# Optimization experiments

Hardware: AMD Instinct MI355X
Metric: run time of the kernel (lower is better)

## Reference

```python
import jax, jax.numpy as jnp
import numpy as np

LN_EPS = 1e-5


def setup_inputs() -> dict:
    key = jax.random.key(0)
    k_h, k_s, k_d, k_w = jax.random.split(key, 4)
    N, E, F_IN, F_OUT = 100000, 1600000, 128, 128
    h = jax.random.normal(k_h, (N, F_IN), dtype=jnp.float32)
    src = jax.random.randint(k_s, (E,), 0, N, dtype=jnp.int32)
    dst = jax.random.randint(k_d, (E,), 0, N, dtype=jnp.int32)
    # Linear(2*in_feats, out_feats): weight [out, 2*in], bias [out]
    W = jax.random.normal(k_w, (F_OUT, 2 * F_IN), dtype=jnp.float32) * (1.0 / np.sqrt(2 * F_IN))
    b = jnp.zeros((F_OUT,), dtype=jnp.float32)
    gamma = jnp.ones((F_OUT,), dtype=jnp.float32)
    beta = jnp.zeros((F_OUT,), dtype=jnp.float32)
    return {"h": h, "src": src, "dst": dst, "W": W, "b": b, "gamma": gamma, "beta": beta}


def reference(h, src, dst, W, b, gamma, beta):
    N = h.shape[0]
    # mean aggregation: update_all(copy_src('h','m'), mean('m','h'))
    msg_sum = jax.ops.segment_sum(h[src], dst, num_segments=N)          # [N, F]
    deg = jax.ops.segment_sum(jnp.ones_like(dst, dtype=h.dtype), dst, num_segments=N)  # [N]
    ah = msg_sum / jnp.maximum(deg, 1.0)[:, None]                        # zero-degree -> 0 (DGL mean gives 0)
    # concat + linear
    hc = jnp.concatenate([h, ah], axis=1)                                # [N, 2F]
    z = hc @ W.T + b                                                     # [N, out]
    # LayerNorm (elementwise affine)
    mu = jnp.mean(z, axis=-1, keepdims=True)
    var = jnp.mean((z - mu) ** 2, axis=-1, keepdims=True)
    z = (z - mu) * jax.lax.rsqrt(var + LN_EPS) * gamma + beta
    # activation = relu
    return jax.nn.relu(z)
```

## Files before the change

### kernel.cpp

```cpp
#include <hip/hip_runtime.h>
#include <stdint.h>

#define FDIM 128
#define NBITS 7
#define BNODES 128
#define CAP 3072
#define PBATCH 8192

typedef __attribute__((ext_vector_type(8))) short bf16x8;
typedef __attribute__((ext_vector_type(4))) float f32x4;
typedef __attribute__((ext_vector_type(8))) unsigned short u16x8;

__device__ __forceinline__ unsigned short f32_to_bf16(float f) {
  union { float f; uint32_t u; } v; v.f = f;
  uint32_t u = v.u;
  u += 0x7FFFu + ((u >> 16) & 1u);
  return (unsigned short)(u >> 16);
}
__device__ __forceinline__ float bf16_to_f32(unsigned short h) {
  union { uint32_t u; float f; } v; v.u = ((uint32_t)h) << 16;
  return v.f;
}

__device__ __forceinline__ void gload_lds16(const void* g, void* l) {
  __builtin_amdgcn_global_load_lds(
      (const __attribute__((address_space(1))) void*)g,
      (__attribute__((address_space(3))) void*)l, 16, 0, 0);
}

__global__ void zero_i32(int* p, int n) {
  int i = blockIdx.x * blockDim.x + threadIdx.x;
  if (i < n) p[i] = 0;
}

__global__ void cvt_bf16_8(const float* __restrict__ in, unsigned short* __restrict__ o, int n8) {
  int i = blockIdx.x * blockDim.x + threadIdx.x;
  if (i >= n8) return;
  float4 a = ((const float4*)in)[i * 2], b = ((const float4*)in)[i * 2 + 1];
  u16x8 r;
  r[0] = f32_to_bf16(a.x); r[1] = f32_to_bf16(a.y); r[2] = f32_to_bf16(a.z); r[3] = f32_to_bf16(a.w);
  r[4] = f32_to_bf16(b.x); r[5] = f32_to_bf16(b.y); r[6] = f32_to_bf16(b.z); r[7] = f32_to_bf16(b.w);
  ((u16x8*)o)[i] = r;
}

__global__ __launch_bounds__(256) void partition_edges(
    const int* __restrict__ src, const int* __restrict__ dst,
    int* __restrict__ gcur, int2* __restrict__ pairs, int E, int nbk) {
  __shared__ int hist[800];
  for (int k = threadIdx.x; k < nbk; k += 256) hist[k] = 0;
  __syncthreads();
  int base = blockIdx.x * PBATCH;
#pragma unroll
  for (int j = 0; j < PBATCH / 256; ++j) {
    int i = base + j * 256 + threadIdx.x;
    if (i < E) atomicAdd(&hist[dst[i] >> NBITS], 1);
  }
  __syncthreads();
  for (int k = threadIdx.x; k < nbk; k += 256) {
    int c = hist[k];
    hist[k] = (c > 0) ? atomicAdd(&gcur[k], c) : 0;
  }
  __syncthreads();
#pragma unroll
  for (int j = 0; j < PBATCH / 256; ++j) {
    int i = base + j * 256 + threadIdx.x;
    if (i < E) {
      int d = dst[i];
      int b = d >> NBITS;
      int pos = atomicAdd(&hist[b], 1);
      if (pos < CAP) pairs[(size_t)b * CAP + pos] = make_int2(src[i], d);
    }
  }
}

__global__ __launch_bounds__(256) void sort_aggregate(
    const unsigned short* __restrict__ h2, const int* __restrict__ gcur,
    const int2* __restrict__ pairs, unsigned short* __restrict__ ah2, int N) {
  __shared__ int cnt[BNODES];
  __shared__ int off[BNODES];
  __shared__ int cur[BNODES];
  __shared__ int lsrc[CAP];
  int b = blockIdx.x;
  int n0 = b << NBITS;
  int tid = threadIdx.x;
  int ec = gcur[b]; if (ec > CAP) ec = CAP;
  for (int k = tid; k < BNODES; k += 256) cnt[k] = 0;
  __syncthreads();
  const int2* pb = pairs + (size_t)b * CAP;
  for (int e = tid; e < ec; e += 256) atomicAdd(&cnt[pb[e].y & (BNODES - 1)], 1);
  __syncthreads();
  if (tid < BNODES) off[tid] = cnt[tid];
  __syncthreads();
  for (int s = 1; s < BNODES; s <<= 1) {
    int v = 0;
    if (tid < BNODES && tid >= s) v = off[tid - s];
    __syncthreads();
    if (tid < BNODES) off[tid] += v;
    __syncthreads();
  }
  if (tid < BNODES) { int e0 = off[tid] - cnt[tid]; off[tid] = e0; cur[tid] = e0; }
  __syncthreads();
  for (int e = tid; e < ec; e += 256) {
    int2 p = pb[e];
    int pos = atomicAdd(&cur[p.y & (BNODES - 1)], 1);
    lsrc[pos] = p.x;
  }
  __syncthreads();
  int g = tid >> 4, lane = tid & 15;
  for (int ln = g; ln < BNODES; ln += 16) {
    int node = n0 + ln;
    if (node >= N) break;
    int s0 = off[ln], d = cnt[ln];
    float acc[8] = {0.f, 0.f, 0.f, 0.f, 0.f, 0.f, 0.f, 0.f};
    for (int e = s0; e < s0 + d; ++e) {
      int sn = lsrc[e];
      u16x8 v = *(const u16x8*)(h2 + (size_t)sn * 128 + lane * 8);
#pragma unroll
      for (int j = 0; j < 8; ++j) acc[j] += bf16_to_f32(v[j]);
    }
    float inv = 1.0f / (float)(d > 0 ? d : 1);
    u16x8 r;
#pragma unroll
    for (int j = 0; j < 8; ++j) r[j] = f32_to_bf16(acc[j] * inv);
    *(u16x8*)(ah2 + (size_t)node * 128 + lane * 8) = r;
  }
}

__global__ __launch_bounds__(256) void gemm_mfma_ln_relu(
    const unsigned short* __restrict__ h2, const unsigned short* __restrict__ ah2,
    const unsigned short* __restrict__ W2, const float* __restrict__ bias,
    const float* __restrict__ gamma, const float* __restrict__ beta,
    float* __restrict__ out, int N) {
  __shared__ unsigned short As[128 * 64];
  __shared__ unsigned short Ws[128 * 64];
  int tid = threadIdx.x;
  int w = tid >> 6, l = tid & 63;
  int lr = l & 15, lg = l >> 4;
  int n0 = blockIdx.x * 128;

  f32x4 acc[2][8];
#pragma unroll
  for (int rt = 0; rt < 2; ++rt)
#pragma unroll
    for (int ct = 0; ct < 8; ++ct) acc[rt][ct] = (f32x4){0.f, 0.f, 0.f, 0.f};

  for (int kt = 0; kt < 4; ++kt) {
    const unsigned short* abase = (kt < 2) ? h2 : ah2;
#pragma unroll
    for (int rd = 0; rd < 4; ++rd) {
      int off = rd * 4096 + tid * 16;
      int r = off >> 7;
      int s = (off >> 4) & 7;
      int ls = s ^ (r & 7);
      int gn = n0 + r; if (gn > N - 1) gn = N - 1;
      gload_lds16((const char*)abase + (size_t)gn * 256 + (size_t)(kt & 1) * 128 + ls * 16,
                  (char*)As + off);
      gload_lds16((const char*)W2 + (size_t)r * 512 + (size_t)kt * 128 + ls * 16,
                  (char*)Ws + off);
    }
    __syncthreads();

    bf16x8 aF[2][2], bF[8][2];
#pragma unroll
    for (int rt = 0; rt < 2; ++rt)
#pragma unroll
      for (int kc = 0; kc < 2; ++kc) {
        int r = w * 32 + rt * 16 + lr;
        int slot = kc * 4 + lg;
        aF[rt][kc] = *(const bf16x8*)((const char*)As + r * 128 + ((slot ^ (r & 7)) * 16));
      }
#pragma unroll
    for (int ct = 0; ct < 8; ++ct)
#pragma unroll
      for (int kc = 0; kc < 2; ++kc) {
        int r = ct * 16 + lr;
        int slot = kc * 4 + lg;
        bF[ct][kc] = *(const bf16x8*)((const char*)Ws + r * 128 + ((slot ^ (r & 7)) * 16));
      }
#pragma unroll
    for (int rt = 0; rt < 2; ++rt)
#pragma unroll
      for (int ct = 0; ct < 8; ++ct)
#pragma unroll
        for (int kc = 0; kc < 2; ++kc)
          acc[rt][ct] = __builtin_amdgcn_mfma_f32_16x16x32_bf16(
              aF[rt][kc], bF[ct][kc], acc[rt][ct], 0, 0, 0);
    __syncthreads();
  }

  float bj[8], gj[8], tj[8];
#pragma unroll
  for (int ct = 0; ct < 8; ++ct) {
    int c = ct * 16 + lr;
    bj[ct] = bias[c]; gj[ct] = gamma[c]; tj[ct] = beta[c];
  }
#pragma unroll
  for (int rt = 0; rt < 2; ++rt)
#pragma unroll
    for (int q = 0; q < 4; ++q) {
      int n = n0 + w * 32 + rt * 16 + lg * 4 + q;
      float v[8], s = 0.f, s2 = 0.f;
#pragma unroll
      for (int ct = 0; ct < 8; ++ct) {
        v[ct] = acc[rt][ct][q] + bj[ct];
        s += v[ct]; s2 += v[ct] * v[ct];
      }
#pragma unroll
      for (int off = 1; off < 16; off <<= 1) {
        s  += __shfl_xor(s, off);
        s2 += __shfl_xor(s2, off);
      }
      float mean = s * (1.f / 128.f);
      float var = s2 * (1.f / 128.f) - mean * mean;
      float rstd = rsqrtf(var + 1e-5f);
      if (n < N) {
#pragma unroll
        for (int ct = 0; ct < 8; ++ct) {
          float o = (v[ct] - mean) * rstd * gj[ct] + tj[ct];
          out[(size_t)n * FDIM + ct * 16 + lr] = fmaxf(o, 0.f);
        }
      }
    }
}

extern "C" void kernel_launch(void* const* d_in, const int* in_sizes, int n_in,
                              void* d_out, int out_size, void* d_ws, size_t ws_size,
                              hipStream_t stream) {
  const float* h     = (const float*)d_in[0];
  const int*   src   = (const int*)d_in[1];
  const int*   dst   = (const int*)d_in[2];
  const float* W     = (const float*)d_in[3];
  const float* bias  = (const float*)d_in[4];
  const float* gamma = (const float*)d_in[5];
  const float* beta  = (const float*)d_in[6];
  float* out = (float*)d_out;
  int N = in_sizes[0] / FDIM;
  int E = in_sizes[1];
  int nbk = (N + BNODES - 1) >> NBITS;

  int* gcur = (int*)d_ws;
  int2* pairs = (int2*)((char*)d_ws + 4096);
  unsigned short* h2  = (unsigned short*)((char*)pairs + (size_t)nbk * CAP * 8);
  unsigned short* ah2 = h2 + (size_t)N * 128;
  unsigned short* W2  = ah2 + (size_t)N * 128;

  zero_i32<<<(nbk + 255) / 256, 256, 0, stream>>>(gcur, nbk);
  cvt_bf16_8<<<(N * FDIM / 8 + 255) / 256, 256, 0, stream>>>(h, h2, N * FDIM / 8);
  cvt_bf16_8<<<(FDIM * 2 * FDIM / 8 + 255) / 256, 256, 0, stream>>>(W, W2, FDIM * 2 * FDIM / 8);
  partition_edges<<<(E + PBATCH - 1) / PBATCH, 256, 0, stream>>>(src, dst, gcur, pairs, E, nbk);
  sort_aggregate<<<nbk, 256, 0, stream>>>(h2, gcur, pairs, ah2, N);
  gemm_mfma_ln_relu<<<(N + 127) / 128, 256, 0, stream>>>(h2, ah2, W2, bias, gamma, beta, out, N);
}
```

Measured before the change: 270.0 us.

## Pack edge pairs into 32-bit words, shrink buckets, vectorize partition, unroll gather

Halves the bucket size to 64 nodes and packs each edge's source id and local destination into one 32-bit word, halving the traffic for the partitioned pairs. The partition kernel reads src/dst as int4 vectors, and the aggregation loop gathers four neighbor rows at a time into independent accumulators to raise memory-level parallelism. This adds more aggregation blocks and a larger shared histogram. The packing relies on node ids fitting in 26 bits, and the vector loads assume 16-byte aligned edge arrays.

After: 224.6 us. 1.2x faster.

```diff
diff --git a/kernel.cpp b/kernel.cpp
--- a/kernel.cpp
+++ b/kernel.cpp
@@ -2,9 +2,9 @@
 #include <stdint.h>
 
 #define FDIM 128
-#define NBITS 7
-#define BNODES 128
-#define CAP 3072
+#define NBITS 6
+#define BNODES 64
+#define CAP 1536
 #define PBATCH 8192
 
 typedef __attribute__((ext_vector_type(8))) short bf16x8;
@@ -45,15 +45,25 @@
 
 __global__ __launch_bounds__(256) void partition_edges(
     const int* __restrict__ src, const int* __restrict__ dst,
-    int* __restrict__ gcur, int2* __restrict__ pairs, int E, int nbk) {
-  __shared__ int hist[800];
+    int* __restrict__ gcur, unsigned int* __restrict__ pairs, int E, int nbk) {
+  __shared__ int hist[1600];
   for (int k = threadIdx.x; k < nbk; k += 256) hist[k] = 0;
   __syncthreads();
   int base = blockIdx.x * PBATCH;
-#pragma unroll
-  for (int j = 0; j < PBATCH / 256; ++j) {
-    int i = base + j * 256 + threadIdx.x;
-    if (i < E) atomicAdd(&hist[dst[i] >> NBITS], 1);
+  const int4* d4p = (const int4*)(dst + base);
+  const int4* s4p = (const int4*)(src + base);
+  int nvec = PBATCH / 4;
+#pragma unroll
+  for (int j = 0; j < PBATCH / 1024; ++j) {
+    int vi = j * 256 + threadIdx.x;
+    int i0 = base + vi * 4;
+    if (i0 < E) {
+      int4 d = d4p[vi];
+      atomicAdd(&hist[d.x >> NBITS], 1);
+      if (i0 + 1 < E) atomicAdd(&hist[d.y >> NBITS], 1);
+      if (i0 + 2 < E) atomicAdd(&hist[d.z >> NBITS], 1);
+      if (i0 + 3 < E) atomicAdd(&hist[d.w >> NBITS], 1);
+    }
   }
   __syncthreads();
   for (int k = threadIdx.x; k < nbk; k += 256) {
@@ -62,20 +72,29 @@
   }
   __syncthreads();
 #pragma unroll
-  for (int j = 0; j < PBATCH / 256; ++j) {
-    int i = base + j * 256 + threadIdx.x;
-    if (i < E) {
-      int d = dst[i];
-      int b = d >> NBITS;
-      int pos = atomicAdd(&hist[b], 1);
-      if (pos < CAP) pairs[(size_t)b * CAP + pos] = make_int2(src[i], d);
+  for (int j = 0; j < PBATCH / 1024; ++j) {
+    int vi = j * 256 + threadIdx.x;
+    int i0 = base + vi * 4;
+    if (i0 < E) {
+      int4 d = d4p[vi];
+      int4 s = s4p[vi];
+#pragma unroll
+      for (int q = 0; q < 4; ++q) {
+        if (i0 + q >= E) break;
+        int dd = (q == 0) ? d.x : (q == 1) ? d.y : (q == 2) ? d.z : d.w;
+        int ss = (q == 0) ? s.x : (q == 1) ? s.y : (q == 2) ? s.z : s.w;
+        int b = dd >> NBITS;
+        int pos = atomicAdd(&hist[b], 1);
+        if (pos < CAP)
+          pairs[(size_t)b * CAP + pos] = ((unsigned)ss << NBITS) | (unsigned)(dd & (BNODES - 1));
+      }
     }
   }
 }
 
 __global__ __launch_bounds__(256) void sort_aggregate(
     const unsigned short* __restrict__ h2, const int* __restrict__ gcur,
-    const int2* __restrict__ pairs, unsigned short* __restrict__ ah2, int N) {
+    const unsigned int* __restrict__ pairs, unsigned short* __restrict__ ah2, int N) {
   __shared__ int cnt[BNODES];
   __shared__ int off[BNODES];
   __shared__ int cur[BNODES];
@@ -84,10 +103,10 @@
   int n0 = b << NBITS;
   int tid = threadIdx.x;
   int ec = gcur[b]; if (ec > CAP) ec = CAP;
-  for (int k = tid; k < BNODES; k += 256) cnt[k] = 0;
-  __syncthreads();
-  const int2* pb = pairs + (size_t)b * CAP;
-  for (int e = tid; e < ec; e += 256) atomicAdd(&cnt[pb[e].y & (BNODES - 1)], 1);
+  if (tid < BNODES) cnt[tid] = 0;
+  __syncthreads();
+  const unsigned int* pb = pairs + (size_t)b * CAP;
+  for (int e = tid; e < ec; e += 256) atomicAdd(&cnt[pb[e] & (BNODES - 1)], 1);
   __syncthreads();
   if (tid < BNODES) off[tid] = cnt[tid];
   __syncthreads();
@@ -101,9 +120,9 @@
   if (tid < BNODES) { int e0 = off[tid] - cnt[tid]; off[tid] = e0; cur[tid] = e0; }
   __syncthreads();
   for (int e = tid; e < ec; e += 256) {
-    int2 p = pb[e];
-    int pos = atomicAdd(&cur[p.y & (BNODES - 1)], 1);
-    lsrc[pos] = p.x;
+    unsigned int p = pb[e];
+    int pos = atomicAdd(&cur[p & (BNODES - 1)], 1);
+    lsrc[pos] = (int)(p >> NBITS);
   }
   __syncthreads();
   int g = tid >> 4, lane = tid & 15;
@@ -111,17 +130,30 @@
     int node = n0 + ln;
     if (node >= N) break;
     int s0 = off[ln], d = cnt[ln];
-    float acc[8] = {0.f, 0.f, 0.f, 0.f, 0.f, 0.f, 0.f, 0.f};
-    for (int e = s0; e < s0 + d; ++e) {
-      int sn = lsrc[e];
-      u16x8 v = *(const u16x8*)(h2 + (size_t)sn * 128 + lane * 8);
-#pragma unroll
-      for (int j = 0; j < 8; ++j) acc[j] += bf16_to_f32(v[j]);
+    int e = s0, eend = s0 + d;
+    float a0[8] = {0,0,0,0,0,0,0,0}, a1[8] = {0,0,0,0,0,0,0,0};
+    float a2[8] = {0,0,0,0,0,0,0,0}, a3[8] = {0,0,0,0,0,0,0,0};
+    for (; e + 4 <= eend; e += 4) {
+      u16x8 v0 = *(const u16x8*)(h2 + (size_t)lsrc[e]     * 128 + lane * 8);
+      u16x8 v1 = *(const u16x8*)(h2 + (size_t)lsrc[e + 1] * 128 + lane * 8);
+      u16x8 v2 = *(const u16x8*)(h2 + (size_t)lsrc[e + 2] * 128 + lane * 8);
+      u16x8 v3 = *(const u16x8*)(h2 + (size_t)lsrc[e + 3] * 128 + lane * 8);
+#pragma unroll
+      for (int j = 0; j < 8; ++j) {
+        a0[j] += bf16_to_f32(v0[j]); a1[j] += bf16_to_f32(v1[j]);
+        a2[j] += bf16_to_f32(v2[j]); a3[j] += bf16_to_f32(v3[j]);
+      }
+    }
+    for (; e < eend; ++e) {
+      u16x8 v = *(const u16x8*)(h2 + (size_t)lsrc[e] * 128 + lane * 8);
+#pragma unroll
+      for (int j = 0; j < 8; ++j) a0[j] += bf16_to_f32(v[j]);
     }
     float inv = 1.0f / (float)(d > 0 ? d : 1);
     u16x8 r;
 #pragma unroll
-    for (int j = 0; j < 8; ++j) r[j] = f32_to_bf16(acc[j] * inv);
+    for (int j = 0; j < 8; ++j)
+      r[j] = f32_to_bf16(((a0[j] + a1[j]) + (a2[j] + a3[j])) * inv);
     *(u16x8*)(ah2 + (size_t)node * 128 + lane * 8) = r;
   }
 }
@@ -239,8 +271,8 @@
   int nbk = (N + BNODES - 1) >> NBITS;
 
   int* gcur = (int*)d_ws;
-  int2* pairs = (int2*)((char*)d_ws + 4096);
-  unsigned short* h2  = (unsigned short*)((char*)pairs + (size_t)nbk * CAP * 8);
+  unsigned int* pairs = (unsigned int*)((char*)d_ws + 8192);
+  unsigned short* h2  = (unsigned short*)((char*)pairs + (size_t)nbk * CAP * 4);
   unsigned short* ah2 = h2 + (size_t)N * 128;
   unsigned short* W2  = ah2 + (size_t)N * 128;
 
```
